# Kernel optimization log

Hardware: AMD Instinct MI355X
Metric: run time of the kernel (lower is better)

Reference implementation:

```python
import jax, jax.numpy as jnp
import numpy as np

B, K, C, H, W = 32, 4, 256, 32, 32
MID = 32  # ceil((C//8)/8)*8
EPS = 1e-5


def setup_inputs() -> dict:
    key = jax.random.key(0)
    ks = jax.random.split(key, 8)
    scale1 = 1.0 / np.sqrt((K + 1) * C)
    scale2 = 1.0 / np.sqrt(MID)
    return {
        "y": jax.random.normal(ks[0], (B, C, H, W), jnp.float32),
        "x0": jax.random.normal(ks[1], (B, C, H, W), jnp.float32),
        "x1": jax.random.normal(ks[2], (B, C, H, W), jnp.float32),
        "x2": jax.random.normal(ks[3], (B, C, H, W), jnp.float32),
        "x3": jax.random.normal(ks[4], (B, C, H, W), jnp.float32),
        "conv1_w": jax.random.normal(ks[5], (MID, (K + 1) * C), jnp.float32) * scale1,
        "bn_gamma": jnp.ones((MID,), jnp.float32),
        "bn_beta": jnp.zeros((MID,), jnp.float32),
        "bn_mean": jnp.zeros((MID,), jnp.float32),
        "bn_var": jnp.ones((MID,), jnp.float32),
        "conv2_w": jax.random.normal(ks[6], ((K + 1) * C, MID), jnp.float32) * scale2,
        "conv2_b": jnp.zeros(((K + 1) * C,), jnp.float32),
    }


def reference(y, x0, x1, x2, x3, conv1_w, bn_gamma, bn_beta, bn_mean, bn_var, conv2_w, conv2_b):
    # Stack K branch feature maps: [B, K, C, H, W]
    xs = jnp.stack([x0, x1, x2, x3], axis=1)
    # Global-average-pooled gate features (1x1 spatial -> plain vectors)
    m_y = jnp.mean(y, axis=(2, 3))            # [B, C]
    m_x = jnp.mean(xs, axis=(3, 4))           # [B, K, C]
    feats = jnp.concatenate([m_y[:, None, :], m_x], axis=1).reshape(B, (K + 1) * C)
    # 1x1 conv -> BN (inference) -> ReLU -> 1x1 conv (all on 1x1 spatial = GEMM)
    h = feats @ conv1_w.T                      # [B, MID]
    h = (h - bn_mean) * (bn_gamma / jnp.sqrt(bn_var + EPS)) + bn_beta
    h = jax.nn.relu(h)
    w = (h @ conv2_w.T + conv2_b).reshape(B, K + 1, C)
    w1 = jax.nn.sigmoid(w[:, 0])               # [B, C] self gate
    w2 = jax.nn.softmax(w[:, 1:], axis=1)      # [B, K, C] branch gates (softmax over K)
    # Gated weighted sum of branches (GatedFunction.forward)
    z = jnp.einsum('bkc,bkchw->bchw', w2, xs)
    return y * w1[:, :, None, None] + z
```

## Files before the change

### kernel.cpp

```cpp
#include <hip/hip_runtime.h>
#include <math.h>

#define B 32
#define K 4
#define C 256
#define HW 1024
#define NT 5
#define MID 32
#define FEAT 1280
#define EPS 1e-5f

__global__ __launch_bounds__(256) void mean_kernel(
    const float* __restrict__ y,
    const float* __restrict__ x0, const float* __restrict__ x1,
    const float* __restrict__ x2, const float* __restrict__ x3,
    float* __restrict__ feats)
{
    int wave = (blockIdx.x << 2) + (threadIdx.x >> 6);
    int lane = threadIdx.x & 63;
    int t   = wave / (B * C);
    int rem = wave - t * (B * C);
    int b   = rem >> 8;
    int c   = rem & 255;
    const float* src = (t == 0) ? y : (t == 1) ? x0 : (t == 2) ? x1
                                    : (t == 3) ? x2 : x3;
    const float4* p = (const float4*)(src + (size_t)(b * C + c) * HW);
    float4 v0 = p[lane];
    float4 v1 = p[lane + 64];
    float4 v2 = p[lane + 128];
    float4 v3 = p[lane + 192];
    float s = v0.x + v0.y + v0.z + v0.w
            + v1.x + v1.y + v1.z + v1.w
            + v2.x + v2.y + v2.z + v2.w
            + v3.x + v3.y + v3.z + v3.w;
#pragma unroll
    for (int m = 32; m >= 1; m >>= 1) s += __shfl_xor(s, m);
    if (lane == 0) feats[b * FEAT + t * C + c] = s * (1.0f / 1024.0f);
}

__global__ __launch_bounds__(256) void gate_kernel(
    const float* __restrict__ feats,
    const float* __restrict__ conv1_w,
    const float* __restrict__ bn_gamma, const float* __restrict__ bn_beta,
    const float* __restrict__ bn_mean,  const float* __restrict__ bn_var,
    const float* __restrict__ conv2_w,
    const float* __restrict__ conv2_b,
    float* __restrict__ gates)
{
    __shared__ float feats_s[FEAT];
    __shared__ float partial[256];
    __shared__ float h_s[MID];

    const int b   = blockIdx.x;
    const int tid = threadIdx.x;

#pragma unroll
    for (int r = 0; r < 5; ++r)
        feats_s[tid + r * 256] = feats[b * FEAT + tid + r * 256];
    __syncthreads();

    const int m = tid & 31;
    const int g = tid >> 5;
    const float4* wrow = (const float4*)(conv1_w + m * FEAT + g * 160);
    float acc = 0.f;
#pragma unroll
    for (int i = 0; i < 40; ++i) {
        float4 wv = wrow[i];
        int j = g * 160 + i * 4;
        acc += wv.x * feats_s[j]     + wv.y * feats_s[j + 1]
             + wv.z * feats_s[j + 2] + wv.w * feats_s[j + 3];
    }
    partial[tid] = acc;
    __syncthreads();
    if (tid < 128) partial[tid] += partial[tid + 128];
    __syncthreads();
    if (tid < 64)  partial[tid] += partial[tid + 64];
    __syncthreads();
    if (tid < 32) {
        float hv  = partial[tid] + partial[tid + 32];
        float inv = rsqrtf(bn_var[tid] + EPS);
        hv = (hv - bn_mean[tid]) * (bn_gamma[tid] * inv) + bn_beta[tid];
        h_s[tid] = fmaxf(hv, 0.f);
    }
    __syncthreads();

    float wv[5];
#pragma unroll
    for (int r = 0; r < 5; ++r) {
        const int j = r * 256 + tid;
        const float4* w2 = (const float4*)(conv2_w + j * MID);
        float a = conv2_b[j];
#pragma unroll
        for (int i = 0; i < 8; ++i) {
            float4 q = w2[i];
            a += q.x * h_s[i * 4]     + q.y * h_s[i * 4 + 1]
               + q.z * h_s[i * 4 + 2] + q.w * h_s[i * 4 + 3];
        }
        wv[r] = a;
    }
    const float w1 = 1.f / (1.f + expf(-wv[0]));
    const float mx = fmaxf(fmaxf(wv[1], wv[2]), fmaxf(wv[3], wv[4]));
    const float e1 = expf(wv[1] - mx), e2 = expf(wv[2] - mx);
    const float e3 = expf(wv[3] - mx), e4 = expf(wv[4] - mx);
    const float inv = 1.f / (e1 + e2 + e3 + e4);
    gates[b * FEAT +        tid] = w1;
    gates[b * FEAT +  256 + tid] = e1 * inv;
    gates[b * FEAT +  512 + tid] = e2 * inv;
    gates[b * FEAT +  768 + tid] = e3 * inv;
    gates[b * FEAT + 1024 + tid] = e4 * inv;
}

__global__ __launch_bounds__(256) void out_kernel(
    const float* __restrict__ y,
    const float* __restrict__ x0, const float* __restrict__ x1,
    const float* __restrict__ x2, const float* __restrict__ x3,
    const float* __restrict__ gates,
    float* __restrict__ out)
{
    const int bc = blockIdx.x;
    const int b  = bc >> 8;
    const int c  = bc & 255;
    const float g0 = gates[b * FEAT +        c];
    const float g1 = gates[b * FEAT +  256 + c];
    const float g2 = gates[b * FEAT +  512 + c];
    const float g3 = gates[b * FEAT +  768 + c];
    const float g4 = gates[b * FEAT + 1024 + c];

    const size_t base = (size_t)bc * HW;
    const int i = threadIdx.x;
    float4 vy = ((const float4*)(y  + base))[i];
    float4 v0 = ((const float4*)(x0 + base))[i];
    float4 v1 = ((const float4*)(x1 + base))[i];
    float4 v2 = ((const float4*)(x2 + base))[i];
    float4 v3 = ((const float4*)(x3 + base))[i];
    float4 r;
    r.x = vy.x * g0 + v0.x * g1 + v1.x * g2 + v2.x * g3 + v3.x * g4;
    r.y = vy.y * g0 + v0.y * g1 + v1.y * g2 + v2.y * g3 + v3.y * g4;
    r.z = vy.z * g0 + v0.z * g1 + v1.z * g2 + v2.z * g3 + v3.z * g4;
    r.w = vy.w * g0 + v0.w * g1 + v1.w * g2 + v2.w * g3 + v3.w * g4;
    ((float4*)(out + base))[i] = r;
}

extern "C" void kernel_launch(void* const* d_in, const int* in_sizes, int n_in,
                              void* d_out, int out_size, void* d_ws, size_t ws_size,
                              hipStream_t stream) {
    const float* y        = (const float*)d_in[0];
    const float* x0       = (const float*)d_in[1];
    const float* x1       = (const float*)d_in[2];
    const float* x2       = (const float*)d_in[3];
    const float* x3       = (const float*)d_in[4];
    const float* conv1_w  = (const float*)d_in[5];
    const float* bn_gamma = (const float*)d_in[6];
    const float* bn_beta  = (const float*)d_in[7];
    const float* bn_mean  = (const float*)d_in[8];
    const float* bn_var   = (const float*)d_in[9];
    const float* conv2_w  = (const float*)d_in[10];
    const float* conv2_b  = (const float*)d_in[11];

    float* feats = (float*)d_ws;
    float* gates = feats + B * FEAT;
    float* out   = (float*)d_out;

    mean_kernel<<<(NT * B * C) / 4, 256, 0, stream>>>(y, x0, x1, x2, x3, feats);
    gate_kernel<<<B, 256, 0, stream>>>(feats, conv1_w, bn_gamma, bn_beta,
                                       bn_mean, bn_var, conv2_w, conv2_b, gates);
    out_kernel<<<B * C, 256, 0, stream>>>(y, x0, x1, x2, x3, gates, out);
}
```

Before: 232.7 us.

## Increase per-wave work in mean, gate, and output kernels

The mean kernel now has each wave reduce four channels, issuing 16 float4 loads per lane and writing one float4 result. The gate kernel moves to 512 threads, with each wave computing four conv1 rows by wave-level shuffle reductions instead of a shared-memory tree. The output kernel now processes two channel slices per block with two float4 loads per input per thread. The aim is more memory-level parallelism, fewer blocks and fewer barriers, at the cost of more registers and lower occupancy.

```diff
diff --git a/kernel.cpp b/kernel.cpp
--- a/kernel.cpp
+++ b/kernel.cpp
@@ -16,29 +16,47 @@
     const float* __restrict__ x2, const float* __restrict__ x3,
     float* __restrict__ feats)
 {
-    int wave = (blockIdx.x << 2) + (threadIdx.x >> 6);
-    int lane = threadIdx.x & 63;
-    int t   = wave / (B * C);
-    int rem = wave - t * (B * C);
-    int b   = rem >> 8;
-    int c   = rem & 255;
+    const int wave = (blockIdx.x << 2) + (threadIdx.x >> 6);
+    const int lane = threadIdx.x & 63;
+    const int t    = wave >> 11;
+    const int rem  = wave & 2047;
+    const int b    = rem >> 6;
+    const int g    = rem & 63;
     const float* src = (t == 0) ? y : (t == 1) ? x0 : (t == 2) ? x1
                                     : (t == 3) ? x2 : x3;
-    const float4* p = (const float4*)(src + (size_t)(b * C + c) * HW);
-    float4 v0 = p[lane];
-    float4 v1 = p[lane + 64];
-    float4 v2 = p[lane + 128];
-    float4 v3 = p[lane + 192];
-    float s = v0.x + v0.y + v0.z + v0.w
-            + v1.x + v1.y + v1.z + v1.w
-            + v2.x + v2.y + v2.z + v2.w
-            + v3.x + v3.y + v3.z + v3.w;
-#pragma unroll
-    for (int m = 32; m >= 1; m >>= 1) s += __shfl_xor(s, m);
-    if (lane == 0) feats[b * FEAT + t * C + c] = s * (1.0f / 1024.0f);
-}
-
-__global__ __launch_bounds__(256) void gate_kernel(
+    const float4* p = (const float4*)(src + ((size_t)(b * C) + g * 4) * HW);
+
+    float4 v[4][4];
+#pragma unroll
+    for (int s = 0; s < 4; ++s)
+#pragma unroll
+        for (int j = 0; j < 4; ++j)
+            v[s][j] = p[s * 256 + j * 64 + lane];
+
+    float s0 = 0.f, s1 = 0.f, s2 = 0.f, s3 = 0.f;
+#pragma unroll
+    for (int j = 0; j < 4; ++j) {
+        s0 += v[0][j].x + v[0][j].y + v[0][j].z + v[0][j].w;
+        s1 += v[1][j].x + v[1][j].y + v[1][j].z + v[1][j].w;
+        s2 += v[2][j].x + v[2][j].y + v[2][j].z + v[2][j].w;
+        s3 += v[3][j].x + v[3][j].y + v[3][j].z + v[3][j].w;
+    }
+#pragma unroll
+    for (int m = 32; m >= 1; m >>= 1) {
+        s0 += __shfl_xor(s0, m);
+        s1 += __shfl_xor(s1, m);
+        s2 += __shfl_xor(s2, m);
+        s3 += __shfl_xor(s3, m);
+    }
+    if (lane == 0) {
+        float4 r = make_float4(s0, s1, s2, s3);
+        r.x *= (1.0f / 1024.0f); r.y *= (1.0f / 1024.0f);
+        r.z *= (1.0f / 1024.0f); r.w *= (1.0f / 1024.0f);
+        *((float4*)&feats[b * FEAT + t * C + g * 4]) = r;
+    }
+}
+
+__global__ __launch_bounds__(512) void gate_kernel(
     const float* __restrict__ feats,
     const float* __restrict__ conv1_w,
     const float* __restrict__ bn_gamma, const float* __restrict__ bn_beta,
@@ -47,67 +65,79 @@
     const float* __restrict__ conv2_b,
     float* __restrict__ gates)
 {
-    __shared__ float feats_s[FEAT];
-    __shared__ float partial[256];
+    __shared__ __align__(16) float feats_s[FEAT];
     __shared__ float h_s[MID];
 
-    const int b   = blockIdx.x;
-    const int tid = threadIdx.x;
-
-#pragma unroll
-    for (int r = 0; r < 5; ++r)
-        feats_s[tid + r * 256] = feats[b * FEAT + tid + r * 256];
+    const int b    = blockIdx.x;
+    const int tid  = threadIdx.x;
+    const int wave = tid >> 6;
+    const int lane = tid & 63;
+
+    for (int i = tid; i < FEAT; i += 512) feats_s[i] = feats[b * FEAT + i];
     __syncthreads();
 
-    const int m = tid & 31;
-    const int g = tid >> 5;
-    const float4* wrow = (const float4*)(conv1_w + m * FEAT + g * 160);
-    float acc = 0.f;
-#pragma unroll
-    for (int i = 0; i < 40; ++i) {
-        float4 wv = wrow[i];
-        int j = g * 160 + i * 4;
-        acc += wv.x * feats_s[j]     + wv.y * feats_s[j + 1]
-             + wv.z * feats_s[j + 2] + wv.w * feats_s[j + 3];
-    }
-    partial[tid] = acc;
+    const float4* fs = (const float4*)feats_s;
+    float4 wv[4][5];
+#pragma unroll
+    for (int r = 0; r < 4; ++r) {
+        const float4* wp = (const float4*)(conv1_w + (wave * 4 + r) * FEAT);
+#pragma unroll
+        for (int k = 0; k < 5; ++k) wv[r][k] = wp[lane + 64 * k];
+    }
+    float a0 = 0.f, a1 = 0.f, a2 = 0.f, a3 = 0.f;
+#pragma unroll
+    for (int k = 0; k < 5; ++k) {
+        float4 f = fs[lane + 64 * k];
+        a0 += wv[0][k].x * f.x + wv[0][k].y * f.y + wv[0][k].z * f.z + wv[0][k].w * f.w;
+        a1 += wv[1][k].x * f.x + wv[1][k].y * f.y + wv[1][k].z * f.z + wv[1][k].w * f.w;
+        a2 += wv[2][k].x * f.x + wv[2][k].y * f.y + wv[2][k].z * f.z + wv[2][k].w * f.w;
+        a3 += wv[3][k].x * f.x + wv[3][k].y * f.y + wv[3][k].z * f.z + wv[3][k].w * f.w;
+    }
+#pragma unroll
+    for (int m = 32; m >= 1; m >>= 1) {
+        a0 += __shfl_xor(a0, m);
+        a1 += __shfl_xor(a1, m);
+        a2 += __shfl_xor(a2, m);
+        a3 += __shfl_xor(a3, m);
+    }
+    if (lane == 0) {
+        float acc[4] = {a0, a1, a2, a3};
+#pragma unroll
+        for (int r = 0; r < 4; ++r) {
+            const int m = wave * 4 + r;
+            float inv = rsqrtf(bn_var[m] + EPS);
+            float hv  = (acc[r] - bn_mean[m]) * (bn_gamma[m] * inv) + bn_beta[m];
+            h_s[m] = fmaxf(hv, 0.f);
+        }
+    }
     __syncthreads();
-    if (tid < 128) partial[tid] += partial[tid + 128];
-    __syncthreads();
-    if (tid < 64)  partial[tid] += partial[tid + 64];
-    __syncthreads();
-    if (tid < 32) {
-        float hv  = partial[tid] + partial[tid + 32];
-        float inv = rsqrtf(bn_var[tid] + EPS);
-        hv = (hv - bn_mean[tid]) * (bn_gamma[tid] * inv) + bn_beta[tid];
-        h_s[tid] = fmaxf(hv, 0.f);
-    }
-    __syncthreads();
-
-    float wv[5];
-#pragma unroll
-    for (int r = 0; r < 5; ++r) {
-        const int j = r * 256 + tid;
-        const float4* w2 = (const float4*)(conv2_w + j * MID);
-        float a = conv2_b[j];
-#pragma unroll
-        for (int i = 0; i < 8; ++i) {
-            float4 q = w2[i];
-            a += q.x * h_s[i * 4]     + q.y * h_s[i * 4 + 1]
-               + q.z * h_s[i * 4 + 2] + q.w * h_s[i * 4 + 3];
+
+    if (tid < 256) {
+        float wvout[5];
+#pragma unroll
+        for (int r = 0; r < 5; ++r) {
+            const int j = r * 256 + tid;
+            const float4* w2 = (const float4*)(conv2_w + j * MID);
+            float a = conv2_b[j];
+#pragma unroll
+            for (int i = 0; i < 8; ++i) {
+                float4 q = w2[i];
+                a += q.x * h_s[i * 4]     + q.y * h_s[i * 4 + 1]
+                   + q.z * h_s[i * 4 + 2] + q.w * h_s[i * 4 + 3];
+            }
+            wvout[r] = a;
         }
-        wv[r] = a;
-    }
-    const float w1 = 1.f / (1.f + expf(-wv[0]));
-    const float mx = fmaxf(fmaxf(wv[1], wv[2]), fmaxf(wv[3], wv[4]));
-    const float e1 = expf(wv[1] - mx), e2 = expf(wv[2] - mx);
-    const float e3 = expf(wv[3] - mx), e4 = expf(wv[4] - mx);
-    const float inv = 1.f / (e1 + e2 + e3 + e4);
-    gates[b * FEAT +        tid] = w1;
-    gates[b * FEAT +  256 + tid] = e1 * inv;
-    gates[b * FEAT +  512 + tid] = e2 * inv;
-    gates[b * FEAT +  768 + tid] = e3 * inv;
-    gates[b * FEAT + 1024 + tid] = e4 * inv;
+        const float w1 = 1.f / (1.f + expf(-wvout[0]));
+        const float mx = fmaxf(fmaxf(wvout[1], wvout[2]), fmaxf(wvout[3], wvout[4]));
+        const float e1 = expf(wvout[1] - mx), e2 = expf(wvout[2] - mx);
+        const float e3 = expf(wvout[3] - mx), e4 = expf(wvout[4] - mx);
+        const float inv = 1.f / (e1 + e2 + e3 + e4);
+        gates[b * FEAT +        tid] = w1;
+        gates[b * FEAT +  256 + tid] = e1 * inv;
+        gates[b * FEAT +  512 + tid] = e2 * inv;
+        gates[b * FEAT +  768 + tid] = e3 * inv;
+        gates[b * FEAT + 1024 + tid] = e4 * inv;
+    }
 }
 
 __global__ __launch_bounds__(256) void out_kernel(
@@ -117,28 +147,44 @@
     const float* __restrict__ gates,
     float* __restrict__ out)
 {
-    const int bc = blockIdx.x;
-    const int b  = bc >> 8;
-    const int c  = bc & 255;
+    const int half  = threadIdx.x >> 7;
+    const int idx   = threadIdx.x & 127;
+    const int slice = blockIdx.x * 2 + half;
+    const int b     = slice >> 8;
+    const int c     = slice & 255;
+
     const float g0 = gates[b * FEAT +        c];
     const float g1 = gates[b * FEAT +  256 + c];
     const float g2 = gates[b * FEAT +  512 + c];
     const float g3 = gates[b * FEAT +  768 + c];
     const float g4 = gates[b * FEAT + 1024 + c];
 
-    const size_t base = (size_t)bc * HW;
-    const int i = threadIdx.x;
-    float4 vy = ((const float4*)(y  + base))[i];
-    float4 v0 = ((const float4*)(x0 + base))[i];
-    float4 v1 = ((const float4*)(x1 + base))[i];
-    float4 v2 = ((const float4*)(x2 + base))[i];
-    float4 v3 = ((const float4*)(x3 + base))[i];
-    float4 r;
-    r.x = vy.x * g0 + v0.x * g1 + v1.x * g2 + v2.x * g3 + v3.x * g4;
-    r.y = vy.y * g0 + v0.y * g1 + v1.y * g2 + v2.y * g3 + v3.y * g4;
-    r.z = vy.z * g0 + v0.z * g1 + v1.z * g2 + v2.z * g3 + v3.z * g4;
-    r.w = vy.w * g0 + v0.w * g1 + v1.w * g2 + v2.w * g3 + v3.w * g4;
-    ((float4*)(out + base))[i] = r;
+    const size_t base = (size_t)slice * HW;
+    const float4* py = (const float4*)(y  + base);
+    const float4* p0 = (const float4*)(x0 + base);
+    const float4* p1 = (const float4*)(x1 + base);
+    const float4* p2 = (const float4*)(x2 + base);
+    const float4* p3 = (const float4*)(x3 + base);
+
+    float4 ya = py[idx], yb = py[idx + 128];
+    float4 aa = p0[idx], ab = p0[idx + 128];
+    float4 ba = p1[idx], bb = p1[idx + 128];
+    float4 ca = p2[idx], cb = p2[idx + 128];
+    float4 da = p3[idx], db = p3[idx + 128];
+
+    float4 r0, r1;
+    r0.x = ya.x * g0 + aa.x * g1 + ba.x * g2 + ca.x * g3 + da.x * g4;
+    r0.y = ya.y * g0 + aa.y * g1 + ba.y * g2 + ca.y * g3 + da.y * g4;
+    r0.z = ya.z * g0 + aa.z * g1 + ba.z * g2 + ca.z * g3 + da.z * g4;
+    r0.w = ya.w * g0 + aa.w * g1 + ba.w * g2 + ca.w * g3 + da.w * g4;
+    r1.x = yb.x * g0 + ab.x * g1 + bb.x * g2 + cb.x * g3 + db.x * g4;
+    r1.y = yb.y * g0 + ab.y * g1 + bb.y * g2 + cb.y * g3 + db.y * g4;
+    r1.z = yb.z * g0 + ab.z * g1 + bb.z * g2 + cb.z * g3 + db.z * g4;
+    r1.w = yb.w * g0 + ab.w * g1 + bb.w * g2 + cb.w * g3 + db.w * g4;
+
+    float4* po = (float4*)(out + base);
+    po[idx]       = r0;
+    po[idx + 128] = r1;
 }
 
 extern "C" void kernel_launch(void* const* d_in, const int* in_sizes, int n_in,
@@ -161,8 +207,8 @@
     float* gates = feats + B * FEAT;
     float* out   = (float*)d_out;
 
-    mean_kernel<<<(NT * B * C) / 4, 256, 0, stream>>>(y, x0, x1, x2, x3, feats);
-    gate_kernel<<<B, 256, 0, stream>>>(feats, conv1_w, bn_gamma, bn_beta,
+    mean_kernel<<<(NT * B * C / 4) / 4, 256, 0, stream>>>(y, x0, x1, x2, x3, feats);
+    gate_kernel<<<B, 512, 0, stream>>>(feats, conv1_w, bn_gamma, bn_beta,
                                        bn_mean, bn_var, conv2_w, conv2_b, gates);
-    out_kernel<<<B * C, 256, 0, stream>>>(y, x0, x1, x2, x3, gates, out);
-}
+    out_kernel<<<B * C / 2, 256, 0, stream>>>(y, x0, x1, x2, x3, gates, out);
+}
```

New measurement: 233.9 us. No clear change (+0.5%).
